# Kernel tuning notes

Hardware: AMD Instinct MI355X
Metric: run time of the kernel (lower is better)

## Reference

```python
import jax, jax.numpy as jnp
import numpy as np

NUM_NODES = 100000


def setup_inputs() -> dict:
    key = jax.random.key(0)
    k1, k2, k3, k4, k5 = jax.random.split(key, 5)
    E = 3200000
    features = jax.random.normal(k1, (NUM_NODES, 32), dtype=jnp.float32)
    edge_srcs = jax.random.randint(k2, (E,), 0, NUM_NODES, dtype=jnp.int32)
    edge_dsts = jax.random.randint(k3, (E,), 0, NUM_NODES, dtype=jnp.int32)
    edge_weights = jax.random.uniform(k4, (E,), dtype=jnp.float32)
    kernels = jax.random.normal(k5, (32, 32), dtype=jnp.float32) * 0.1
    biases = jnp.zeros((32,), dtype=jnp.float32)
    return {
        "features": features,
        "edge_srcs": edge_srcs,
        "edge_dsts": edge_dsts,
        "edge_weights": edge_weights,
        "kernels": kernels,
        "biases": biases,
    }


def reference(features, edge_srcs, edge_dsts, edge_weights, kernels, biases):
    num_nodes = features.shape[0]
    # dense transform: [N, F_in] @ [F_in, F_out] -> [N, F_out]
    h = features @ kernels
    # per-src degrees via segment sum of ones, clipped to >= 1
    deg = jax.ops.segment_sum(
        jnp.ones_like(edge_srcs, dtype=h.dtype), edge_srcs, num_segments=num_nodes
    )
    norm = jnp.clip(deg, 1.0, None) ** -0.5  # [N]
    # symmetric-normalized edge weights: norm[src] * w * norm[dst]
    w = norm[edge_srcs] * edge_weights * norm[edge_dsts]  # [E]
    # gather dst features, scale, scatter-add into src rows
    nbr = h[edge_dsts] * w[:, None]  # [E, F_out]
    reduced = jax.ops.segment_sum(nbr, edge_srcs, num_segments=num_nodes)
    return reduced + biases
```

## Files before the change

### kernel.cpp

```cpp
#include <hip/hip_runtime.h>

#define FDIM 32
#define BSH 7
#define BNODES 128
#define NBMAX 1024
#define CHUNK 8192
#define NCMAX 512
#define CAP 4608
#define NGRAN 160

typedef unsigned int u32;
typedef unsigned short u16;

#define BFLO(u) __uint_as_float((u) << 16)
#define BFHI(u) __uint_as_float((u) & 0xFFFF0000u)

__device__ __forceinline__ void acc8(float4& p0, float4& p1, float w, uint4 h) {
    p0.x = fmaf(w, BFLO(h.x), p0.x);
    p0.y = fmaf(w, BFHI(h.x), p0.y);
    p0.z = fmaf(w, BFLO(h.y), p0.z);
    p0.w = fmaf(w, BFHI(h.y), p0.w);
    p1.x = fmaf(w, BFLO(h.z), p1.x);
    p1.y = fmaf(w, BFHI(h.z), p1.y);
    p1.z = fmaf(w, BFLO(h.w), p1.z);
    p1.w = fmaf(w, BFHI(h.w), p1.w);
}

__global__ __launch_bounds__(1024) void k1b(const int* __restrict__ srcs,
                                            const int* __restrict__ dsts,
                                            const float* __restrict__ ew,
                                            u32* __restrict__ offsT,
                                            u32* __restrict__ rkey,
                                            float* __restrict__ rw,
                                            int E, int NB, int nch) {
    __shared__ u32 lh[NBMAX];
    __shared__ u32 wsum[16];
    int t = threadIdx.x, c = blockIdx.x;
    int base = c * CHUNK;
    int end = base + CHUNK; if (end > E) end = E;
    int nloc = end - base;
    for (int i = t; i < NB; i += 1024) lh[i] = 0u;
    __syncthreads();
    int i0 = t * 8;
    bool full = (i0 + 8 <= nloc);
    int sv[8];
    if (full) {
        int4 a = ((const int4*)(srcs + base))[t * 2];
        int4 bb = ((const int4*)(srcs + base))[t * 2 + 1];
        sv[0] = a.x; sv[1] = a.y; sv[2] = a.z; sv[3] = a.w;
        sv[4] = bb.x; sv[5] = bb.y; sv[6] = bb.z; sv[7] = bb.w;
#pragma unroll
        for (int k = 0; k < 8; ++k) atomicAdd(&lh[sv[k] >> BSH], 1u);
    } else {
        for (int i = i0; i < i0 + 8 && i < nloc; ++i) {
            int s = srcs[base + i];
            sv[i - i0] = s;
            atomicAdd(&lh[s >> BSH], 1u);
        }
    }
    __syncthreads();
    int lane = t & 63, w = t >> 6;
    u32 v = (t < NB) ? lh[t] : 0u;
    u32 inc = v;
#pragma unroll
    for (int d = 1; d < 64; d <<= 1) {
        u32 o = __shfl_up(inc, (unsigned)d, 64);
        if (lane >= d) inc += o;
    }
    if (lane == 63) wsum[w] = inc;
    __syncthreads();
    u32 woff = 0;
    for (int i = 0; i < w; ++i) woff += wsum[i];
    inc += woff;
    u32 ex = inc - v;
    if (t < NB) { offsT[(size_t)t * nch + c] = ex; lh[t] = ex; }
    if (t == 0) offsT[(size_t)NB * nch + c] = (u32)nloc;
    __syncthreads();
    if (full) {
        int4 d0 = ((const int4*)(dsts + base))[t * 2];
        int4 d1 = ((const int4*)(dsts + base))[t * 2 + 1];
        float4 w0 = ((const float4*)(ew + base))[t * 2];
        float4 w1 = ((const float4*)(ew + base))[t * 2 + 1];
        int dv[8] = { d0.x, d0.y, d0.z, d0.w, d1.x, d1.y, d1.z, d1.w };
        float wv[8] = { w0.x, w0.y, w0.z, w0.w, w1.x, w1.y, w1.z, w1.w };
#pragma unroll
        for (int k = 0; k < 8; ++k) {
            int s = sv[k];
            u32 pos = atomicAdd(&lh[s >> BSH], 1u);
            rkey[(size_t)base + pos] = ((u32)(s & (BNODES - 1)) << 17) | (u32)dv[k];
            rw[(size_t)base + pos] = wv[k];
        }
    } else {
        for (int i = i0; i < i0 + 8 && i < nloc; ++i) {
            int s = sv[i - i0];
            u32 pos = atomicAdd(&lh[s >> BSH], 1u);
            rkey[(size_t)base + pos] = ((u32)(s & (BNODES - 1)) << 17) | (u32)dsts[base + i];
            rw[(size_t)base + pos] = ew[base + i];
        }
    }
}

__global__ __launch_bounds__(512) void k_nh(const u32* __restrict__ rkey,
                                            const u32* __restrict__ offsT,
                                            const float* __restrict__ feat,
                                            const float* __restrict__ kern,
                                            u16* __restrict__ hsb,
                                            u32* __restrict__ nodemeta,
                                            int N, int NB, int nch) {
    __shared__ float skern[FDIM * FDIM];
    __shared__ float sfeat[BNODES * FDIM];
    __shared__ u32 sstart[NCMAX];
    __shared__ u32 ltmp[NCMAX];
    __shared__ u16 lut[NGRAN];
    __shared__ u32 lcnt[BNODES];
    __shared__ float lnorm[BNODES];
    __shared__ u32 wsum[8];
    __shared__ u32 ws2[2];
    int b = blockIdx.x, t = threadIdx.x;
    for (int i = t; i < FDIM * FDIM; i += 512) skern[i] = kern[i];
    int base_n = b << BSH;
    int base_nf = base_n * FDIM;
    int lim = N * FDIM - base_nf; if (lim > BNODES * FDIM) lim = BNODES * FDIM;
    for (int i = t; i < lim; i += 512) sfeat[i] = feat[base_nf + i];
    if (t < BNODES) lcnt[t] = 0u;
    u32 rl = 0u;
    if (t < nch) {
        u32 s0 = offsT[(size_t)b * nch + t];
        u32 s1 = offsT[(size_t)(b + 1) * nch + t];
        sstart[t] = s0;
        rl = s1 - s0;
    }
    int lane = t & 63, w = t >> 6;
    u32 inc = rl;
#pragma unroll
    for (int d = 1; d < 64; d <<= 1) {
        u32 o = __shfl_up(inc, (unsigned)d, 64);
        if (lane >= d) inc += o;
    }
    if (lane == 63) wsum[w] = inc;
    __syncthreads();
    u32 woff = 0;
    for (int i = 0; i < w; ++i) woff += wsum[i];
    inc += woff;
    ltmp[t] = inc;
    __syncthreads();
    u32 tot = ltmp[nch - 1];
    if (tot > CAP) tot = CAP;
    if (t < NGRAN && (u32)(t << 5) < tot) {
        u32 target = (u32)t << 5;
        int lo = 0, hi = nch - 1;
        while (lo < hi) { int m = (lo + hi) >> 1; if (ltmp[m] > target) hi = m; else lo = m + 1; }
        lut[t] = (u16)lo;
    }
    __syncthreads();
    for (u32 g = t; g < tot; g += 512) {
        int r = lut[g >> 5];
        while (ltmp[r] <= g) ++r;
        u32 pl0 = r ? ltmp[r - 1] : 0u;
        u32 key = rkey[(size_t)r * CHUNK + sstart[r] + (g - pl0)];
        atomicAdd(&lcnt[key >> 17], 1u);
    }
    __syncthreads();
    u32 d = 0u, pad = 0u, inc2 = 0u;
    if (t < BNODES) {
        d = lcnt[t];
        pad = (d + 1u) & ~1u;
        inc2 = pad;
    }
    if (t < 128) {
#pragma unroll
        for (int dd = 1; dd < 64; dd <<= 1) {
            u32 o = __shfl_up(inc2, (unsigned)dd, 64);
            if ((t & 63) >= dd) inc2 += o;
        }
        if ((t & 63) == 63) ws2[t >> 6] = inc2;
    }
    __syncthreads();
    if (t < 128) {
        if (t >= 64) inc2 += ws2[0];
        u32 ex = inc2 - pad;
        lnorm[t] = rsqrtf(fmaxf((float)d, 1.0f));
        int n = base_n + t;
        if (n < N) nodemeta[n] = ex | (d << 16);
    }
    __syncthreads();
    int f = t & 31, g8 = t >> 5;
    for (int k8 = 0; k8 < 8; ++k8) {
        int nl = g8 * 8 + k8;
        int n = base_n + nl;
        if (n >= N) continue;
        float acc = 0.f;
#pragma unroll
        for (int k = 0; k < FDIM; ++k)
            acc = fmaf(sfeat[nl * FDIM + k], skern[k * FDIM + f], acc);
        float x = lnorm[nl] * acc;
        u32 u = __float_as_uint(x);
        u = (u + 0x7FFFu + ((u >> 16) & 1u)) >> 16;
        hsb[(size_t)n * FDIM + f] = (u16)u;
    }
}

__global__ __launch_bounds__(512) void k2(const u32* __restrict__ rkey,
                                          const float* __restrict__ rw,
                                          const u32* __restrict__ offsT,
                                          const u32* __restrict__ nodemeta,
                                          const u16* __restrict__ hsb,
                                          const float* __restrict__ bias,
                                          float* __restrict__ out,
                                          int N, int NB, int nch) {
    __shared__ uint2 ssrec[CAP];
    __shared__ u32 sstart[NCMAX];
    __shared__ u32 ltmp[NCMAX];
    __shared__ u16 lut[NGRAN];
    __shared__ u32 loff[BNODES];
    __shared__ u32 lcnt[BNODES];
    __shared__ u32 lcur[BNODES];
    __shared__ u32 snode[BNODES];
    __shared__ u32 lbin[128];
    __shared__ u32 wsum[8];
    __shared__ u32 ws2[2];
    int b = blockIdx.x, t = threadIdx.x;
    int base_n = b << BSH;
    if (t < BNODES) {
        int n = base_n + t;
        u32 m = (n < N) ? nodemeta[n] : 0u;
        loff[t] = m & 0xFFFFu;
        lcnt[t] = m >> 16;
        lcur[t] = m & 0xFFFFu;
    }
    if (t < 128) lbin[t] = 0u;
    u32 rl = 0u;
    if (t < nch) {
        u32 s0 = offsT[(size_t)b * nch + t];
        u32 s1 = offsT[(size_t)(b + 1) * nch + t];
        sstart[t] = s0;
        rl = s1 - s0;
    }
    int lane = t & 63, w = t >> 6;
    u32 inc = rl;
#pragma unroll
    for (int d = 1; d < 64; d <<= 1) {
        u32 o = __shfl_up(inc, (unsigned)d, 64);
        if (lane >= d) inc += o;
    }
    if (lane == 63) wsum[w] = inc;
    __syncthreads();
    u32 woff = 0;
    for (int i = 0; i < w; ++i) woff += wsum[i];
    inc += woff;
    ltmp[t] = inc;
    __syncthreads();
    u32 tot = ltmp[nch - 1];
    if (tot > CAP) tot = CAP;
    if (t < NGRAN && (u32)(t << 5) < tot) {
        u32 target = (u32)t << 5;
        int lo = 0, hi = nch - 1;
        while (lo < hi) { int m = (lo + hi) >> 1; if (ltmp[m] > target) hi = m; else lo = m + 1; }
        lut[t] = (u16)lo;
    }
    __syncthreads();
    for (u32 g2 = t; g2 < tot; g2 += 512) {
        int r = lut[g2 >> 5];
        while (ltmp[r] <= g2) ++r;
        u32 pl0 = r ? ltmp[r - 1] : 0u;
        size_t idx = (size_t)r * CHUNK + sstart[r] + (g2 - pl0);
        u32 key = rkey[idx];
        float wv = rw[idx];
        u32 sl = key >> 17;
        u32 pos = atomicAdd(&lcur[sl], 1u);
        if (pos < CAP) ssrec[pos] = make_uint2(key & 0x1FFFFu, __float_as_uint(wv));
    }
    if (t < BNODES) {
        u32 len = lcnt[t];
        atomicAdd(&lbin[len > 127u ? 127u : len], 1u);
    }
    __syncthreads();
    u32 bv_ = 0u, binc = 0u;
    if (t < 128) {
        bv_ = lbin[t];
        binc = bv_;
#pragma unroll
        for (int dd = 1; dd < 64; dd <<= 1) {
            u32 o = __shfl_up(binc, (unsigned)dd, 64);
            if ((t & 63) >= dd) binc += o;
        }
        if ((t & 63) == 63) ws2[t >> 6] = binc;
    }
    __syncthreads();
    if (t < 128) {
        if (t >= 64) binc += ws2[0];
        lbin[t] = binc - bv_;
    }
    __syncthreads();
    if (t < BNODES) {
        u32 len = lcnt[t];
        u32 pos = atomicAdd(&lbin[len > 127u ? 127u : len], 1u);
        snode[pos] = (u32)t;
    }
    __syncthreads();
    int l = t & 3, g = t >> 2;
    u32 nl = snode[g];
    int n = base_n + (int)nl;
    u32 off = loff[nl];
    u32 len = lcnt[nl];
    float ns = rsqrtf(fmaxf((float)len, 1.0f));
    const uint4* hp4 = (const uint4*)hsb;
    float4 bv0 = ((const float4*)bias)[2 * l];
    float4 bv1 = ((const float4*)bias)[2 * l + 1];
    float4 x0 = make_float4(0.f, 0.f, 0.f, 0.f), x1 = make_float4(0.f, 0.f, 0.f, 0.f);
    float4 y0 = make_float4(0.f, 0.f, 0.f, 0.f), y1 = make_float4(0.f, 0.f, 0.f, 0.f);
    u32 j = 0;
    for (; j + 4 <= len; j += 4) {
        uint4 q0 = *(const uint4*)(ssrec + off + j);
        uint4 q1 = *(const uint4*)(ssrec + off + j + 2);
        uint4 h0 = hp4[(size_t)q0.x * 4 + l];
        uint4 h1 = hp4[(size_t)q0.z * 4 + l];
        uint4 h2 = hp4[(size_t)q1.x * 4 + l];
        uint4 h3 = hp4[(size_t)q1.z * 4 + l];
        float w0 = __uint_as_float(q0.y), w1 = __uint_as_float(q0.w);
        float w2 = __uint_as_float(q1.y), w3 = __uint_as_float(q1.w);
        acc8(x0, x1, w0, h0);
        acc8(y0, y1, w1, h1);
        acc8(x0, x1, w2, h2);
        acc8(y0, y1, w3, h3);
    }
    for (; j < len; ++j) {
        uint2 q = ssrec[off + j];
        uint4 h = hp4[(size_t)q.x * 4 + l];
        acc8(x0, x1, __uint_as_float(q.y), h);
    }
    if (n < N) {
        float4 r0, r1;
        r0.x = fmaf(ns, x0.x + y0.x, bv0.x);
        r0.y = fmaf(ns, x0.y + y0.y, bv0.y);
        r0.z = fmaf(ns, x0.z + y0.z, bv0.z);
        r0.w = fmaf(ns, x0.w + y0.w, bv0.w);
        r1.x = fmaf(ns, x1.x + y1.x, bv1.x);
        r1.y = fmaf(ns, x1.y + y1.y, bv1.y);
        r1.z = fmaf(ns, x1.z + y1.z, bv1.z);
        r1.w = fmaf(ns, x1.w + y1.w, bv1.w);
        ((float4*)(out + (size_t)n * FDIM))[2 * l] = r0;
        ((float4*)(out + (size_t)n * FDIM))[2 * l + 1] = r1;
    }
}

extern "C" void kernel_launch(void* const* d_in, const int* in_sizes, int n_in,
                              void* d_out, int out_size, void* d_ws, size_t ws_size,
                              hipStream_t stream) {
    const float* feat = (const float*)d_in[0];
    const int*   srcs = (const int*)d_in[1];
    const int*   dsts = (const int*)d_in[2];
    const float* ew   = (const float*)d_in[3];
    const float* kern = (const float*)d_in[4];
    const float* bias = (const float*)d_in[5];
    float* out = (float*)d_out;

    int N = in_sizes[0] / FDIM;
    int E = in_sizes[1];
    int NB = (N + BNODES - 1) >> BSH;
    int nchunks = (E + CHUNK - 1) / CHUNK;

    char* w = (char*)d_ws;
    u16* hsb      = (u16*)w;   w += (((size_t)N * FDIM * sizeof(u16) + 15) & ~15ull);
    u32* rkey     = (u32*)w;   w += (size_t)nchunks * CHUNK * sizeof(u32);
    float* rw     = (float*)w; w += (size_t)nchunks * CHUNK * sizeof(float);
    u32* offsT    = (u32*)w;   w += (size_t)(NB + 1) * nchunks * sizeof(u32);
    u32* nodemeta = (u32*)w;   w += (size_t)N * sizeof(u32);

    k1b<<<nchunks, 1024, 0, stream>>>(srcs, dsts, ew, offsT, rkey, rw, E, NB, nchunks);
    k_nh<<<NB, 512, 0, stream>>>(rkey, offsT, feat, kern, hsb, nodemeta, N, NB, nchunks);
    k2<<<NB, 512, 0, stream>>>(rkey, rw, offsT, nodemeta, hsb, bias, out, N, NB, nchunks);
}
```

Before: 206.9 us.

## Pack edge records, reuse local ranks, and batch gathers across kernels

Key and weight now go into one interleaved uint2 record array instead of separate key and weight arrays. The bucketing kernel loads all inputs before its histogram and reuses the rank returned by the first atomic, which removes the second pass of shared atomics. The binary-search lookup table for finding which chunk an edge belongs to is replaced by a per-block run-id table filled directly from the scan, and record loads are batched eight deep to raise memory-level parallelism. Other edits vectorise the feature and kernel staging loads, cache kernel columns in registers for the node transform, and unroll the aggregation gather to eight. The run-id fill is serial per chunk and the extra registers may lower occupancy.

```diff
diff --git a/kernel.cpp b/kernel.cpp
--- a/kernel.cpp
+++ b/kernel.cpp
@@ -7,7 +7,6 @@
 #define CHUNK 8192
 #define NCMAX 512
 #define CAP 4608
-#define NGRAN 160
 
 typedef unsigned int u32;
 typedef unsigned short u16;
@@ -30,8 +29,7 @@
                                             const int* __restrict__ dsts,
                                             const float* __restrict__ ew,
                                             u32* __restrict__ offsT,
-                                            u32* __restrict__ rkey,
-                                            float* __restrict__ rw,
+                                            uint2* __restrict__ rec,
                                             int E, int NB, int nch) {
     __shared__ u32 lh[NBMAX];
     __shared__ u32 wsum[16];
@@ -39,23 +37,41 @@
     int base = c * CHUNK;
     int end = base + CHUNK; if (end > E) end = E;
     int nloc = end - base;
-    for (int i = t; i < NB; i += 1024) lh[i] = 0u;
-    __syncthreads();
     int i0 = t * 8;
     bool full = (i0 + 8 <= nloc);
-    int sv[8];
+    int sv[8], dv[8];
+    float wv[8];
+    u32 rk[8];
     if (full) {
-        int4 a = ((const int4*)(srcs + base))[t * 2];
-        int4 bb = ((const int4*)(srcs + base))[t * 2 + 1];
-        sv[0] = a.x; sv[1] = a.y; sv[2] = a.z; sv[3] = a.w;
-        sv[4] = bb.x; sv[5] = bb.y; sv[6] = bb.z; sv[7] = bb.w;
-#pragma unroll
-        for (int k = 0; k < 8; ++k) atomicAdd(&lh[sv[k] >> BSH], 1u);
+        int4 a  = ((const int4*)(srcs + base))[t * 2];
+        int4 b2 = ((const int4*)(srcs + base))[t * 2 + 1];
+        int4 d0 = ((const int4*)(dsts + base))[t * 2];
+        int4 d1 = ((const int4*)(dsts + base))[t * 2 + 1];
+        float4 w0 = ((const float4*)(ew + base))[t * 2];
+        float4 w1 = ((const float4*)(ew + base))[t * 2 + 1];
+        sv[0]=a.x; sv[1]=a.y; sv[2]=a.z; sv[3]=a.w; sv[4]=b2.x; sv[5]=b2.y; sv[6]=b2.z; sv[7]=b2.w;
+        dv[0]=d0.x; dv[1]=d0.y; dv[2]=d0.z; dv[3]=d0.w; dv[4]=d1.x; dv[5]=d1.y; dv[6]=d1.z; dv[7]=d1.w;
+        wv[0]=w0.x; wv[1]=w0.y; wv[2]=w0.z; wv[3]=w0.w; wv[4]=w1.x; wv[5]=w1.y; wv[6]=w1.z; wv[7]=w1.w;
     } else {
-        for (int i = i0; i < i0 + 8 && i < nloc; ++i) {
-            int s = srcs[base + i];
-            sv[i - i0] = s;
-            atomicAdd(&lh[s >> BSH], 1u);
+#pragma unroll
+        for (int k = 0; k < 8; ++k) {
+            int i = i0 + k;
+            bool v = i < nloc;
+            sv[k] = v ? srcs[base + i] : 0;
+            dv[k] = v ? dsts[base + i] : 0;
+            wv[k] = v ? ew[base + i] : 0.f;
+        }
+    }
+    for (int i = t; i < NB; i += 1024) lh[i] = 0u;
+    __syncthreads();
+    if (full) {
+#pragma unroll
+        for (int k = 0; k < 8; ++k) rk[k] = atomicAdd(&lh[sv[k] >> BSH], 1u);
+    } else {
+#pragma unroll
+        for (int k = 0; k < 8; ++k) {
+            bool v = (i0 + k) < nloc;
+            rk[k] = v ? atomicAdd(&lh[sv[k] >> BSH], 1u) : 0u;
         }
     }
     __syncthreads();
@@ -77,30 +93,27 @@
     if (t == 0) offsT[(size_t)NB * nch + c] = (u32)nloc;
     __syncthreads();
     if (full) {
-        int4 d0 = ((const int4*)(dsts + base))[t * 2];
-        int4 d1 = ((const int4*)(dsts + base))[t * 2 + 1];
-        float4 w0 = ((const float4*)(ew + base))[t * 2];
-        float4 w1 = ((const float4*)(ew + base))[t * 2 + 1];
-        int dv[8] = { d0.x, d0.y, d0.z, d0.w, d1.x, d1.y, d1.z, d1.w };
-        float wv[8] = { w0.x, w0.y, w0.z, w0.w, w1.x, w1.y, w1.z, w1.w };
 #pragma unroll
         for (int k = 0; k < 8; ++k) {
             int s = sv[k];
-            u32 pos = atomicAdd(&lh[s >> BSH], 1u);
-            rkey[(size_t)base + pos] = ((u32)(s & (BNODES - 1)) << 17) | (u32)dv[k];
-            rw[(size_t)base + pos] = wv[k];
+            u32 pos = lh[s >> BSH] + rk[k];
+            rec[(size_t)base + pos] = make_uint2(((u32)(s & (BNODES - 1)) << 17) | (u32)dv[k],
+                                                __float_as_uint(wv[k]));
         }
     } else {
-        for (int i = i0; i < i0 + 8 && i < nloc; ++i) {
-            int s = sv[i - i0];
-            u32 pos = atomicAdd(&lh[s >> BSH], 1u);
-            rkey[(size_t)base + pos] = ((u32)(s & (BNODES - 1)) << 17) | (u32)dsts[base + i];
-            rw[(size_t)base + pos] = ew[base + i];
+#pragma unroll
+        for (int k = 0; k < 8; ++k) {
+            if ((i0 + k) < nloc) {
+                int s = sv[k];
+                u32 pos = lh[s >> BSH] + rk[k];
+                rec[(size_t)base + pos] = make_uint2(((u32)(s & (BNODES - 1)) << 17) | (u32)dv[k],
+                                                    __float_as_uint(wv[k]));
+            }
         }
     }
 }
 
-__global__ __launch_bounds__(512) void k_nh(const u32* __restrict__ rkey,
+__global__ __launch_bounds__(512) void k_nh(const uint2* __restrict__ rec,
                                             const u32* __restrict__ offsT,
                                             const float* __restrict__ feat,
                                             const float* __restrict__ kern,
@@ -109,26 +122,24 @@
                                             int N, int NB, int nch) {
     __shared__ float skern[FDIM * FDIM];
     __shared__ float sfeat[BNODES * FDIM];
-    __shared__ u32 sstart[NCMAX];
-    __shared__ u32 ltmp[NCMAX];
-    __shared__ u16 lut[NGRAN];
+    __shared__ u32 sbase[NCMAX];
+    __shared__ u16 runid[CAP];
     __shared__ u32 lcnt[BNODES];
     __shared__ float lnorm[BNODES];
     __shared__ u32 wsum[8];
     __shared__ u32 ws2[2];
+    __shared__ u32 stot;
     int b = blockIdx.x, t = threadIdx.x;
-    for (int i = t; i < FDIM * FDIM; i += 512) skern[i] = kern[i];
+    for (int i = t; i < FDIM * FDIM / 4; i += 512) ((float4*)skern)[i] = ((const float4*)kern)[i];
     int base_n = b << BSH;
     int base_nf = base_n * FDIM;
     int lim = N * FDIM - base_nf; if (lim > BNODES * FDIM) lim = BNODES * FDIM;
-    for (int i = t; i < lim; i += 512) sfeat[i] = feat[base_nf + i];
+    for (int i = t; i < (lim >> 2); i += 512) ((float4*)sfeat)[i] = ((const float4*)(feat + base_nf))[i];
     if (t < BNODES) lcnt[t] = 0u;
-    u32 rl = 0u;
+    u32 rl = 0u, s0 = 0u;
     if (t < nch) {
-        u32 s0 = offsT[(size_t)b * nch + t];
-        u32 s1 = offsT[(size_t)(b + 1) * nch + t];
-        sstart[t] = s0;
-        rl = s1 - s0;
+        s0 = offsT[(size_t)b * nch + t];
+        rl = offsT[(size_t)(b + 1) * nch + t] - s0;
     }
     int lane = t & 63, w = t >> 6;
     u32 inc = rl;
@@ -142,23 +153,35 @@
     u32 woff = 0;
     for (int i = 0; i < w; ++i) woff += wsum[i];
     inc += woff;
-    ltmp[t] = inc;
-    __syncthreads();
-    u32 tot = ltmp[nch - 1];
-    if (tot > CAP) tot = CAP;
-    if (t < NGRAN && (u32)(t << 5) < tot) {
-        u32 target = (u32)t << 5;
-        int lo = 0, hi = nch - 1;
-        while (lo < hi) { int m = (lo + hi) >> 1; if (ltmp[m] > target) hi = m; else lo = m + 1; }
-        lut[t] = (u16)lo;
-    }
-    __syncthreads();
-    for (u32 g = t; g < tot; g += 512) {
-        int r = lut[g >> 5];
-        while (ltmp[r] <= g) ++r;
-        u32 pl0 = r ? ltmp[r - 1] : 0u;
-        u32 key = rkey[(size_t)r * CHUNK + sstart[r] + (g - pl0)];
-        atomicAdd(&lcnt[key >> 17], 1u);
+    if (t < nch) {
+        u32 pl0 = inc - rl;
+        sbase[t] = (u32)t * CHUNK + s0 - pl0;
+        u32 p = pl0 < CAP ? pl0 : CAP;
+        u32 e = pl0 + rl; if (e > CAP) e = CAP;
+        for (; p < e; ++p) runid[p] = (u16)t;
+    }
+    if (t == nch - 1) stot = inc;
+    __syncthreads();
+    u32 tot = stot; if (tot > CAP) tot = CAP;
+    {
+        u32 keyv[8]; bool val[8];
+#pragma unroll
+        for (int i = 0; i < 8; ++i) {
+            u32 g = (u32)t + ((u32)i << 9);
+            val[i] = g < tot;
+            keyv[i] = 0u;
+            if (val[i]) {
+                int r = runid[g];
+                keyv[i] = rec[(size_t)(sbase[r] + g)].x;
+            }
+        }
+#pragma unroll
+        for (int i = 0; i < 8; ++i)
+            if (val[i]) atomicAdd(&lcnt[keyv[i] >> 17], 1u);
+        for (u32 g = (u32)t + 4096u; g < tot; g += 512u) {
+            int r = runid[g];
+            atomicAdd(&lcnt[rec[(size_t)(sbase[r] + g)].x >> 17], 1u);
+        }
     }
     __syncthreads();
     u32 d = 0u, pad = 0u, inc2 = 0u;
@@ -185,23 +208,33 @@
     }
     __syncthreads();
     int f = t & 31, g8 = t >> 5;
+    float kc[FDIM];
+#pragma unroll
+    for (int k = 0; k < FDIM; ++k) kc[k] = skern[k * FDIM + f];
+#pragma unroll
     for (int k8 = 0; k8 < 8; ++k8) {
         int nl = g8 * 8 + k8;
         int n = base_n + nl;
-        if (n >= N) continue;
+        const float4* fr = (const float4*)(sfeat + nl * FDIM);
+        float4 rr[8];
+#pragma unroll
+        for (int q = 0; q < 8; ++q) rr[q] = fr[q];
         float acc = 0.f;
 #pragma unroll
-        for (int k = 0; k < FDIM; ++k)
-            acc = fmaf(sfeat[nl * FDIM + k], skern[k * FDIM + f], acc);
+        for (int q = 0; q < 8; ++q) {
+            acc = fmaf(rr[q].x, kc[4 * q + 0], acc);
+            acc = fmaf(rr[q].y, kc[4 * q + 1], acc);
+            acc = fmaf(rr[q].z, kc[4 * q + 2], acc);
+            acc = fmaf(rr[q].w, kc[4 * q + 3], acc);
+        }
         float x = lnorm[nl] * acc;
         u32 u = __float_as_uint(x);
         u = (u + 0x7FFFu + ((u >> 16) & 1u)) >> 16;
-        hsb[(size_t)n * FDIM + f] = (u16)u;
+        if (n < N) hsb[(size_t)n * FDIM + f] = (u16)u;
     }
 }
 
-__global__ __launch_bounds__(512) void k2(const u32* __restrict__ rkey,
-                                          const float* __restrict__ rw,
+__global__ __launch_bounds__(512) void k2(const uint2* __restrict__ rec,
                                           const u32* __restrict__ offsT,
                                           const u32* __restrict__ nodemeta,
                                           const u16* __restrict__ hsb,
@@ -209,9 +242,8 @@
                                           float* __restrict__ out,
                                           int N, int NB, int nch) {
     __shared__ uint2 ssrec[CAP];
-    __shared__ u32 sstart[NCMAX];
-    __shared__ u32 ltmp[NCMAX];
-    __shared__ u16 lut[NGRAN];
+    __shared__ u32 sbase[NCMAX];
+    __shared__ u16 runid[CAP];
     __shared__ u32 loff[BNODES];
     __shared__ u32 lcnt[BNODES];
     __shared__ u32 lcur[BNODES];
@@ -219,6 +251,7 @@
     __shared__ u32 lbin[128];
     __shared__ u32 wsum[8];
     __shared__ u32 ws2[2];
+    __shared__ u32 stot;
     int b = blockIdx.x, t = threadIdx.x;
     int base_n = b << BSH;
     if (t < BNODES) {
@@ -229,12 +262,10 @@
         lcur[t] = m & 0xFFFFu;
     }
     if (t < 128) lbin[t] = 0u;
-    u32 rl = 0u;
+    u32 rl = 0u, s0 = 0u;
     if (t < nch) {
-        u32 s0 = offsT[(size_t)b * nch + t];
-        u32 s1 = offsT[(size_t)(b + 1) * nch + t];
-        sstart[t] = s0;
-        rl = s1 - s0;
+        s0 = offsT[(size_t)b * nch + t];
+        rl = offsT[(size_t)(b + 1) * nch + t] - s0;
     }
     int lane = t & 63, w = t >> 6;
     u32 inc = rl;
@@ -248,27 +279,42 @@
     u32 woff = 0;
     for (int i = 0; i < w; ++i) woff += wsum[i];
     inc += woff;
-    ltmp[t] = inc;
-    __syncthreads();
-    u32 tot = ltmp[nch - 1];
-    if (tot > CAP) tot = CAP;
-    if (t < NGRAN && (u32)(t << 5) < tot) {
-        u32 target = (u32)t << 5;
-        int lo = 0, hi = nch - 1;
-        while (lo < hi) { int m = (lo + hi) >> 1; if (ltmp[m] > target) hi = m; else lo = m + 1; }
-        lut[t] = (u16)lo;
-    }
-    __syncthreads();
-    for (u32 g2 = t; g2 < tot; g2 += 512) {
-        int r = lut[g2 >> 5];
-        while (ltmp[r] <= g2) ++r;
-        u32 pl0 = r ? ltmp[r - 1] : 0u;
-        size_t idx = (size_t)r * CHUNK + sstart[r] + (g2 - pl0);
-        u32 key = rkey[idx];
-        float wv = rw[idx];
-        u32 sl = key >> 17;
-        u32 pos = atomicAdd(&lcur[sl], 1u);
-        if (pos < CAP) ssrec[pos] = make_uint2(key & 0x1FFFFu, __float_as_uint(wv));
+    if (t < nch) {
+        u32 pl0 = inc - rl;
+        sbase[t] = (u32)t * CHUNK + s0 - pl0;
+        u32 p = pl0 < CAP ? pl0 : CAP;
+        u32 e = pl0 + rl; if (e > CAP) e = CAP;
+        for (; p < e; ++p) runid[p] = (u16)t;
+    }
+    if (t == nch - 1) stot = inc;
+    __syncthreads();
+    u32 tot = stot; if (tot > CAP) tot = CAP;
+    {
+        uint2 qv[8]; bool val[8];
+#pragma unroll
+        for (int i = 0; i < 8; ++i) {
+            u32 g = (u32)t + ((u32)i << 9);
+            val[i] = g < tot;
+            qv[i] = make_uint2(0u, 0u);
+            if (val[i]) {
+                int r = runid[g];
+                qv[i] = rec[(size_t)(sbase[r] + g)];
+            }
+        }
+#pragma unroll
+        for (int i = 0; i < 8; ++i) {
+            if (val[i]) {
+                u32 sl = qv[i].x >> 17;
+                u32 pos = atomicAdd(&lcur[sl], 1u);
+                if (pos < CAP) ssrec[pos] = make_uint2(qv[i].x & 0x1FFFFu, qv[i].y);
+            }
+        }
+        for (u32 g = (u32)t + 4096u; g < tot; g += 512u) {
+            int r = runid[g];
+            uint2 q = rec[(size_t)(sbase[r] + g)];
+            u32 pos = atomicAdd(&lcur[q.x >> 17], 1u);
+            if (pos < CAP) ssrec[pos] = make_uint2(q.x & 0x1FFFFu, q.y);
+        }
     }
     if (t < BNODES) {
         u32 len = lcnt[t];
@@ -310,6 +356,28 @@
     float4 x0 = make_float4(0.f, 0.f, 0.f, 0.f), x1 = make_float4(0.f, 0.f, 0.f, 0.f);
     float4 y0 = make_float4(0.f, 0.f, 0.f, 0.f), y1 = make_float4(0.f, 0.f, 0.f, 0.f);
     u32 j = 0;
+    for (; j + 8 <= len; j += 8) {
+        uint4 q0 = *(const uint4*)(ssrec + off + j);
+        uint4 q1 = *(const uint4*)(ssrec + off + j + 2);
+        uint4 q2 = *(const uint4*)(ssrec + off + j + 4);
+        uint4 q3 = *(const uint4*)(ssrec + off + j + 6);
+        uint4 h0 = hp4[(size_t)q0.x * 4 + l];
+        uint4 h1 = hp4[(size_t)q0.z * 4 + l];
+        uint4 h2 = hp4[(size_t)q1.x * 4 + l];
+        uint4 h3 = hp4[(size_t)q1.z * 4 + l];
+        uint4 h4 = hp4[(size_t)q2.x * 4 + l];
+        uint4 h5 = hp4[(size_t)q2.z * 4 + l];
+        uint4 h6 = hp4[(size_t)q3.x * 4 + l];
+        uint4 h7 = hp4[(size_t)q3.z * 4 + l];
+        acc8(x0, x1, __uint_as_float(q0.y), h0);
+        acc8(y0, y1, __uint_as_float(q0.w), h1);
+        acc8(x0, x1, __uint_as_float(q1.y), h2);
+        acc8(y0, y1, __uint_as_float(q1.w), h3);
+        acc8(x0, x1, __uint_as_float(q2.y), h4);
+        acc8(y0, y1, __uint_as_float(q2.w), h5);
+        acc8(x0, x1, __uint_as_float(q3.y), h6);
+        acc8(y0, y1, __uint_as_float(q3.w), h7);
+    }
     for (; j + 4 <= len; j += 4) {
         uint4 q0 = *(const uint4*)(ssrec + off + j);
         uint4 q1 = *(const uint4*)(ssrec + off + j + 2);
@@ -317,12 +385,10 @@
         uint4 h1 = hp4[(size_t)q0.z * 4 + l];
         uint4 h2 = hp4[(size_t)q1.x * 4 + l];
         uint4 h3 = hp4[(size_t)q1.z * 4 + l];
-        float w0 = __uint_as_float(q0.y), w1 = __uint_as_float(q0.w);
-        float w2 = __uint_as_float(q1.y), w3 = __uint_as_float(q1.w);
-        acc8(x0, x1, w0, h0);
-        acc8(y0, y1, w1, h1);
-        acc8(x0, x1, w2, h2);
-        acc8(y0, y1, w3, h3);
+        acc8(x0, x1, __uint_as_float(q0.y), h0);
+        acc8(y0, y1, __uint_as_float(q0.w), h1);
+        acc8(x0, x1, __uint_as_float(q1.y), h2);
+        acc8(y0, y1, __uint_as_float(q1.w), h3);
     }
     for (; j < len; ++j) {
         uint2 q = ssrec[off + j];
@@ -362,12 +428,11 @@
 
     char* w = (char*)d_ws;
     u16* hsb      = (u16*)w;   w += (((size_t)N * FDIM * sizeof(u16) + 15) & ~15ull);
-    u32* rkey     = (u32*)w;   w += (size_t)nchunks * CHUNK * sizeof(u32);
-    float* rw     = (float*)w; w += (size_t)nchunks * CHUNK * sizeof(float);
+    uint2* rec    = (uint2*)w; w += (size_t)nchunks * CHUNK * sizeof(uint2);
     u32* offsT    = (u32*)w;   w += (size_t)(NB + 1) * nchunks * sizeof(u32);
     u32* nodemeta = (u32*)w;   w += (size_t)N * sizeof(u32);
 
-    k1b<<<nchunks, 1024, 0, stream>>>(srcs, dsts, ew, offsT, rkey, rw, E, NB, nchunks);
-    k_nh<<<NB, 512, 0, stream>>>(rkey, offsT, feat, kern, hsb, nodemeta, N, NB, nchunks);
-    k2<<<NB, 512, 0, stream>>>(rkey, rw, offsT, nodemeta, hsb, bias, out, N, NB, nchunks);
+    k1b<<<nchunks, 1024, 0, stream>>>(srcs, dsts, ew, offsT, rec, E, NB, nchunks);
+    k_nh<<<NB, 512, 0, stream>>>(rec, offsT, feat, kern, hsb, nodemeta, N, NB, nchunks);
+    k2<<<NB, 512, 0, stream>>>(rec, offsT, nodemeta, hsb, bias, out, N, NB, nchunks);
 }
```

Result: faster. 176.1 us (-14.9%).
